# Optimization experiments

Hardware: AMD Instinct MI355X
Metric: run time of the kernel (lower is better)

## Reference

```python
import jax, jax.numpy as jnp
import numpy as np

DIM = 192
NUM_HEADS = 6
WS = (7, 7, 7)
N_TOK = WS[0] * WS[1] * WS[2]  # 343
TABLE_SIZE = (2 * WS[0] - 1) * (2 * WS[1] - 1) * (2 * WS[2] - 1)  # 2197


def _relative_position_index():
    # faithful replication of the torch buffer construction (incl. its strides)
    coords = np.stack(np.meshgrid(np.arange(WS[0]), np.arange(WS[1]), np.arange(WS[2]), indexing='ij'))
    flat = coords.reshape(3, -1)                     # [3, N]
    rel = flat[:, :, None] - flat[:, None, :]        # [3, N, N]
    rel = rel.transpose(1, 2, 0).astype(np.int64)    # [N, N, 3]
    rel[..., 0] += WS[0] - 1
    rel[..., 1] += WS[1] - 1
    rel[..., 2] += WS[2] - 1
    rel[..., 0] *= 3 * WS[1] - 1  # = 20 (source uses window_size[1] here)
    rel[..., 1] *= 2 * WS[1] - 1  # = 13
    return rel.sum(-1)            # [N, N]


def setup_inputs() -> dict:
    key = jax.random.key(0)
    ks = jax.random.split(key, 10)
    B_, nW = 256, 64
    x1 = jax.random.normal(ks[0], (B_, N_TOK, DIM), dtype=jnp.float32)
    x2 = jax.random.normal(ks[1], (B_, N_TOK, DIM), dtype=jnp.float32)
    mask = jax.random.normal(ks[2], (nW, N_TOK, N_TOK), dtype=jnp.float32)
    table = 0.02 * jax.random.normal(ks[3], (TABLE_SIZE, NUM_HEADS), dtype=jnp.float32)
    s = DIM ** -0.5
    q_w = s * jax.random.normal(ks[4], (DIM, DIM), dtype=jnp.float32)
    q_b = jnp.zeros((DIM,), jnp.float32)
    kv_w = s * jax.random.normal(ks[5], (2 * DIM, DIM), dtype=jnp.float32)
    kv_b = jnp.zeros((2 * DIM,), jnp.float32)
    proj_w = s * jax.random.normal(ks[6], (DIM, DIM), dtype=jnp.float32)
    proj_b = jnp.zeros((DIM,), jnp.float32)
    rel_idx = jnp.asarray(_relative_position_index(), dtype=jnp.int32)
    return {"x1": x1, "x2": x2, "mask": mask, "table": table,
            "q_w": q_w, "q_b": q_b, "kv_w": kv_w, "kv_b": kv_b,
            "proj_w": proj_w, "proj_b": proj_b, "rel_idx": rel_idx}


def reference(x1, x2, mask, table, q_w, q_b, kv_w, kv_b, proj_w, proj_b, rel_idx):
    B_, N, C = x1.shape
    H = NUM_HEADS
    hd = C // H
    scale = hd ** -0.5
    # q from x1, k/v from x2 (isfusion cross-attention path)
    q = (x1 @ q_w.T + q_b).reshape(B_, N, H, hd).transpose(0, 2, 1, 3) * scale  # [B,H,N,hd]
    kv = (x2 @ kv_w.T + kv_b).reshape(B_, N, 2, H, hd).transpose(2, 0, 3, 1, 4)  # [2,B,H,N,hd]
    k, v = kv[0], kv[1]
    attn = jnp.einsum('bhnd,bhmd->bhnm', q, k)  # [B,H,N,N]
    # relative position bias gather -> [H,N,N]
    bias = table[rel_idx.reshape(-1)].reshape(N, N, H).transpose(2, 0, 1)
    attn = attn + bias[None]
    # shifted-window mask add
    nW = mask.shape[0]
    attn = (attn.reshape(B_ // nW, nW, H, N, N) + mask[None, :, None]).reshape(B_, H, N, N)
    attn = jax.nn.softmax(attn, axis=-1)
    out = jnp.einsum('bhnm,bhmd->bnhd', attn, v).reshape(B_, N, C)
    return out @ proj_w.T + proj_b
```

## Files before the change

### kernel.cpp

```cpp
#include <hip/hip_runtime.h>

typedef __attribute__((ext_vector_type(8))) short short8;
typedef __attribute__((ext_vector_type(4))) float f32x4;
typedef __attribute__((ext_vector_type(16))) float f32x16;
typedef __attribute__((ext_vector_type(4))) unsigned short us4;
typedef __attribute__((ext_vector_type(2))) unsigned int u32x2;

#define NTOK 343
#define BMP 352
#define LOG2E 1.4426950408889634f
#define FPLANE 11264
#define WPITCH 200

#define OFF_QG   0u
#define OFF_KG   33718272u
#define OFF_VT   68321280u
#define OFF_AO   102924288u
#define OFF_WB   136642560u

__device__ __forceinline__ unsigned short f2bf(float f) {
  union { float f; unsigned u; } v; v.f = f;
  unsigned r = v.u + 0x7FFFu + ((v.u >> 16) & 1u);
  return (unsigned short)(r >> 16);
}

__device__ __forceinline__ float bf2f(unsigned short b) {
  union { unsigned u; float f; } v; v.u = ((unsigned)b) << 16;
  return v.f;
}

__device__ __forceinline__ short8 ld8(const unsigned short* p) {
  return *reinterpret_cast<const short8*>(p);
}

__device__ __forceinline__ float fexp2(float x) {
  float r; asm("v_exp_f32 %0, %1" : "=v"(r) : "v"(x)); return r;
}

__device__ __forceinline__ unsigned cvtpk(float a, float b) {
  unsigned r; asm("v_cvt_pk_bf16_f32 %0, %1, %2" : "=v"(r) : "v"(a), "v"(b)); return r;
}

__device__ __forceinline__ void plswap(unsigned &a, unsigned &b) {
  asm("v_permlane32_swap_b32 %0, %1" : "+v"(a), "+v"(b));
}

__device__ __forceinline__ f32x16 mfma32(short8 a, short8 b, f32x16 c) {
  return __builtin_amdgcn_mfma_f32_32x32x16_bf16(a, b, c, 0, 0, 0);
}

__device__ __forceinline__ f32x4 mfma16(short8 a, short8 b, f32x4 c) {
  return __builtin_amdgcn_mfma_f32_16x16x32_bf16(a, b, c, 0, 0, 0);
}

union frag_u { unsigned u[4]; short8 s8; };

__global__ __launch_bounds__(256) void precompute(
    const float* __restrict__ x1, const float* __restrict__ x2,
    const float* __restrict__ mask, const float* __restrict__ table,
    const int* __restrict__ rel_idx,
    const float* __restrict__ qw, const float* __restrict__ kvw, const float* __restrict__ pw,
    unsigned short* __restrict__ x1b, unsigned short* __restrict__ x2b,
    unsigned short* __restrict__ wq_bf, unsigned short* __restrict__ wkv_bf,
    unsigned short* __restrict__ wp_bf,
    unsigned short* __restrict__ bias_bf, unsigned short* __restrict__ mask_bf,
    unsigned short* __restrict__ v_frag)
{
  const int idx = blockIdx.x * 256 + threadIdx.x;
  if (idx < 8429568) {
    const float* src; unsigned short* dst; int i;
    if (idx < 4214784) { src = x1; dst = x1b; i = idx; }
    else               { src = x2; dst = x2b; i = idx - 4214784; }
    f32x4 v = *reinterpret_cast<const f32x4*>(src + i * 4);
    us4 o; o[0] = f2bf(v[0]); o[1] = f2bf(v[1]); o[2] = f2bf(v[2]); o[3] = f2bf(v[3]);
    *reinterpret_cast<us4*>(dst + i * 4) = o;
  } else if (idx < 8466432) {
    const int wi = idx - 8429568;
    const float* src; unsigned short* dst; int i;
    if (wi < 9216)       { src = qw;  dst = wq_bf;  i = wi; }
    else if (wi < 27648) { src = kvw; dst = wkv_bf; i = wi - 9216; }
    else                 { src = pw;  dst = wp_bf;  i = wi - 27648; }
    f32x4 v = *reinterpret_cast<const f32x4*>(src + i * 4);
    us4 o; o[0] = f2bf(v[0]); o[1] = f2bf(v[1]); o[2] = f2bf(v[2]); o[3] = f2bf(v[3]);
    *reinterpret_cast<us4*>(dst + i * 4) = o;
  } else if (idx < 10398208) {
    const int mi = idx - 8466432;
    const int row = mi / 88, q = mi - row * 88;
    const int j0 = q * 4;
    unsigned short* dst = mask_bf + row * BMP + j0;
    if (q < 85) {
      const float* src = mask + row * NTOK + j0;
      us4 o; o[0] = f2bf(LOG2E * src[0]); o[1] = f2bf(LOG2E * src[1]);
      o[2] = f2bf(LOG2E * src[2]); o[3] = f2bf(LOG2E * src[3]);
      *reinterpret_cast<us4*>(dst) = o;
    } else {
      us4 o;
      #pragma unroll
      for (int i = 0; i < 4; ++i) {
        const int col = j0 + i;
        o[i] = (col < NTOK) ? f2bf(LOG2E * mask[row * NTOK + col]) : (unsigned short)0;
      }
      *reinterpret_cast<us4*>(dst) = o;
    }
  } else if (idx < 10515857) {
    const int i = idx - 10398208;
    const int ri = rel_idx[i] * 6;
    const int rrow = i / NTOK, j = i - rrow * NTOK;
    unsigned short* dst = bias_bf + rrow * BMP + j;
    #pragma unroll
    for (int h = 0; h < 6; ++h) dst[h * (NTOK * BMP)] = f2bf(LOG2E * table[ri + h]);
  } else if (idx < 10517915) {
    const int p = idx - 10515857;
    unsigned short* dst = bias_bf + p * BMP + NTOK;
    #pragma unroll
    for (int c = 0; c < 9; ++c) dst[c] = 0;
  } else if (idx < 10714523) {
    const int i = idx - 10517915;
    const int bh = i >> 7, c = i & 127;
    short8 z = (short8){0,0,0,0,0,0,0,0};
    *reinterpret_cast<short8*>(v_frag + bh * FPLANE + 10240 + c * 8) = z;
  }
}

__global__ __launch_bounds__(256) void proj(
    const unsigned short* __restrict__ x1b, const unsigned short* __restrict__ x2b,
    const unsigned short* __restrict__ wq_bf, const unsigned short* __restrict__ wkv_bf,
    const float* __restrict__ qb, const float* __restrict__ kvb,
    unsigned short* __restrict__ q_g, unsigned short* __restrict__ k_g,
    unsigned short* __restrict__ v_frag)
{
  __shared__ __align__(16) unsigned short wLds[192 * WPITCH];

  const int tid = threadIdx.x;
  const int wv = tid >> 6, lane = tid & 63, lg = lane >> 4, lr = lane & 15;
  const int path = blockIdx.y;
  const int b = blockIdx.x & 255, seg = blockIdx.x >> 8;
  const int n0 = seg * 128 + wv * 32;

  const unsigned short* X = (path == 0) ? x1b : x2b;
  const unsigned short* Wsrc = (path == 0) ? wq_bf : (path == 1 ? wkv_bf : wkv_bf + 36864);

  #pragma unroll
  for (int i = 0; i < 18; ++i) {
    const int c = i * 256 + tid;
    const int row = c / 24, c8 = c - row * 24;
    *reinterpret_cast<short8*>(&wLds[row * WPITCH + c8 * 8]) = ld8(Wsrc + row * 192 + c8 * 8);
  }
  __syncthreads();

  const int rowbase = b * NTOK;
  const int nA = n0 + lr, nB = n0 + 16 + lr;
  const unsigned short* xr0 = X + (rowbase + (nA < NTOK ? nA : NTOK - 1)) * 192 + lg * 8;
  const unsigned short* xr1 = X + (rowbase + (nB < NTOK ? nB : NTOK - 1)) * 192 + lg * 8;

  short8 ax[2][6];
  #pragma unroll
  for (int kk = 0; kk < 6; ++kk) {
    ax[0][kk] = ld8(xr0 + kk * 32);
    ax[1][kk] = ld8(xr1 + kk * 32);
  }

  f32x4 acc[2][12];
  #pragma unroll
  for (int i = 0; i < 2; ++i)
    #pragma unroll
    for (int j = 0; j < 12; ++j) acc[i][j] = (f32x4){0.f, 0.f, 0.f, 0.f};

  if (path < 2) {
    #pragma unroll
    for (int kk = 0; kk < 6; ++kk) {
      const int k0 = kk * 32 + lg * 8;
      #pragma unroll
      for (int ct = 0; ct < 12; ++ct) {
        const short8 wf = *reinterpret_cast<const short8*>(&wLds[(ct * 16 + lr) * WPITCH + k0]);
        acc[0][ct] = mfma16(wf, ax[0][kk], acc[0][ct]);
        acc[1][ct] = mfma16(wf, ax[1][kk], acc[1][ct]);
      }
    }
    if (path == 0) {
      const float qs = 0.17677669529663687f * LOG2E;
      #pragma unroll
      for (int tt = 0; tt < 2; ++tt) {
        const int n = n0 + tt * 16 + lr;
        if (n < NTOK) {
          unsigned short* ob = q_g + (b * 6 * NTOK + n) * 32;
          #pragma unroll
          for (int ct = 0; ct < 12; ++ct) {
            const f32x4 bb = *reinterpret_cast<const f32x4*>(qb + ct * 16 + lg * 4);
            u32x2 pk;
            pk[0] = cvtpk((acc[tt][ct][0] + bb[0]) * qs, (acc[tt][ct][1] + bb[1]) * qs);
            pk[1] = cvtpk((acc[tt][ct][2] + bb[2]) * qs, (acc[tt][ct][3] + bb[3]) * qs);
            *reinterpret_cast<u32x2*>(ob + (ct >> 1) * (NTOK * 32) + (ct & 1) * 16 + lg * 4) = pk;
          }
        }
      }
    } else {
      #pragma unroll
      for (int tt = 0; tt < 2; ++tt) {
        const int n = n0 + tt * 16 + lr;
        if (n < 352) {
          unsigned short* ob = k_g + b * 6 * FPLANE + (n >> 5) * 1024
                               + ((lg >> 1) * 32 + (n & 31)) * 8 + (lg & 1) * 4;
          #pragma unroll
          for (int ct = 0; ct < 12; ++ct) {
            const f32x4 bb = *reinterpret_cast<const f32x4*>(kvb + ct * 16 + lg * 4);
            u32x2 pk;
            pk[0] = cvtpk(acc[tt][ct][0] + bb[0], acc[tt][ct][1] + bb[1]);
            pk[1] = cvtpk(acc[tt][ct][2] + bb[2], acc[tt][ct][3] + bb[3]);
            *reinterpret_cast<u32x2*>(ob + (ct >> 1) * FPLANE + (ct & 1) * 512) = pk;
          }
        }
      }
    }
  } else {
    #pragma unroll
    for (int kk = 0; kk < 6; ++kk) {
      const int k0 = kk * 32 + lg * 8;
      #pragma unroll
      for (int ct = 0; ct < 12; ++ct) {
        const short8 wf = *reinterpret_cast<const short8*>(&wLds[(ct * 16 + lr) * WPITCH + k0]);
        acc[0][ct] = mfma16(ax[0][kk], wf, acc[0][ct]);
        acc[1][ct] = mfma16(ax[1][kk], wf, acc[1][ct]);
      }
    }
    float bs[12];
    #pragma unroll
    for (int ct = 0; ct < 12; ++ct) bs[ct] = kvb[192 + ct * 16 + lr];
    #pragma unroll
    for (int tt = 0; tt < 2; ++tt) {
      const int nb = n0 + tt * 16 + lg * 4;
      if (nb < 352) {
        unsigned short* vb = v_frag + b * 6 * FPLANE + (nb >> 5) * 1024
                             + ((nb >> 4) & 1) * 512 + ((nb >> 3) & 1) * 256 + (nb & 7);
        #pragma unroll
        for (int ct = 0; ct < 12; ++ct) {
          const int d = (ct & 1) * 16 + lr;
          u32x2 pk;
          pk[0] = cvtpk(acc[tt][ct][0] + bs[ct], acc[tt][ct][1] + bs[ct]);
          pk[1] = cvtpk(acc[tt][ct][2] + bs[ct], acc[tt][ct][3] + bs[ct]);
          *reinterpret_cast<u32x2*>(vb + (ct >> 1) * FPLANE + d * 8) = pk;
        }
      }
    }
  }
}

__global__ __launch_bounds__(256, 3) void attn(
    const unsigned short* __restrict__ q_g, const unsigned short* __restrict__ k_g,
    const unsigned short* __restrict__ v_frag, const unsigned short* __restrict__ bias_bf,
    const unsigned short* __restrict__ mask_bf, unsigned short* __restrict__ attn_out)
{
  __shared__ __align__(16) unsigned short kvlds[2][FPLANE];

  const int tid = threadIdx.x;
  const int wv = tid >> 6, lane = tid & 63;
  const int l31 = lane & 31, hi = lane >> 5;
  const int s0 = blockIdx.x;
  const int xcd = s0 & 7, ii = s0 >> 3;
  const int g = xcd * 48 + (ii >> 2), mem = ii & 3;
  const int h = g >> 6, w = g & 63;
  const int b = mem * 64 + w;
  const int bid = b * 6 + h;

  const unsigned short* qp = q_g + bid * (NTOK * 32);
  const unsigned short* kpf = k_g + bid * FPLANE;
  const unsigned short* vpf = v_frag + bid * FPLANE;
  const unsigned short* bias_h = bias_bf + h * (NTOK * BMP);
  const unsigned short* mask_w = mask_bf + w * (NTOK * BMP);

  #pragma unroll
  for (int j = 0; j < 6; ++j) {
    const int c = j * 256 + tid;
    if (c < 1408) {
      *reinterpret_cast<short8*>(&kvlds[0][c * 8]) = ld8(kpf + c * 8);
      *reinterpret_cast<short8*>(&kvlds[1][c * 8]) = ld8(vpf + c * 8);
    }
  }
  __syncthreads();

  for (int qt = wv; qt < 11; qt += 4) {
    const int qq = qt * 32 + l31;
    const int qrc = qq < NTOK ? qq : NTOK - 1;
    const short8 qf0 = ld8(qp + qrc * 32 + hi * 8);
    const short8 qf1 = ld8(qp + qrc * 32 + 16 + hi * 8);
    const unsigned short* bmb = bias_h + qrc * BMP + hi * 4;
    const unsigned short* bmm = mask_w + qrc * BMP + hi * 4;

    f32x16 O;
    #pragma unroll
    for (int r = 0; r < 16; ++r) O[r] = 0.f;
    f32x4 sacc = (f32x4){0.f, 0.f, 0.f, 0.f};

    us4 nb[4], nm[4];
    #pragma unroll
    for (int gg = 0; gg < 4; ++gg) {
      nb[gg] = *reinterpret_cast<const us4*>(bmb + gg * 8);
      nm[gg] = *reinterpret_cast<const us4*>(bmm + gg * 8);
    }

    #pragma unroll
    for (int kt = 0; kt < 11; ++kt) {
      us4 cb[4], cm[4];
      #pragma unroll
      for (int gg = 0; gg < 4; ++gg) { cb[gg] = nb[gg]; cm[gg] = nm[gg]; }
      if (kt < 10) {
        const int kn = (kt + 1) * 32;
        #pragma unroll
        for (int gg = 0; gg < 4; ++gg) {
          nb[gg] = *reinterpret_cast<const us4*>(bmb + kn + gg * 8);
          nm[gg] = *reinterpret_cast<const us4*>(bmm + kn + gg * 8);
        }
      }

      const short8 kf0 = ld8(&kvlds[0][kt * 1024 + lane * 8]);
      const short8 kf1 = ld8(&kvlds[0][kt * 1024 + 512 + lane * 8]);
      f32x16 sv;
      #pragma unroll
      for (int r = 0; r < 16; ++r) sv[r] = 0.f;
      __builtin_amdgcn_s_setprio(1);
      sv = mfma32(kf0, qf0, sv);
      sv = mfma32(kf1, qf1, sv);
      __builtin_amdgcn_s_setprio(0);

      float p[16];
      #pragma unroll
      for (int gg = 0; gg < 4; ++gg) {
        #pragma unroll
        for (int j = 0; j < 4; ++j) {
          float v = sv[gg * 4 + j] + (bf2f(cb[gg][j]) + bf2f(cm[gg][j]));
          if (kt == 10 && (gg * 8 + hi * 4 + j) >= 23) v = -3.0e38f;
          p[gg * 4 + j] = fexp2(v);
        }
      }
      #pragma unroll
      for (int j = 0; j < 4; ++j)
        sacc[j] += (p[j] + p[4 + j]) + (p[8 + j] + p[12 + j]);

      unsigned c01 = cvtpk(p[0], p[1]),   c23 = cvtpk(p[2], p[3]);
      unsigned c45 = cvtpk(p[4], p[5]),   c67 = cvtpk(p[6], p[7]);
      unsigned d01 = cvtpk(p[8], p[9]),   d23 = cvtpk(p[10], p[11]);
      unsigned d45 = cvtpk(p[12], p[13]), d67 = cvtpk(p[14], p[15]);
      plswap(c01, c45); plswap(c23, c67);
      plswap(d01, d45); plswap(d23, d67);
      frag_u P0, P1;
      P0.u[0] = c01; P0.u[1] = c23; P0.u[2] = c45; P0.u[3] = c67;
      P1.u[0] = d01; P1.u[1] = d23; P1.u[2] = d45; P1.u[3] = d67;

      const short8 vf0 = ld8(&kvlds[1][kt * 1024 + lane * 8]);
      const short8 vf1 = ld8(&kvlds[1][kt * 1024 + 512 + lane * 8]);
      __builtin_amdgcn_s_setprio(1);
      O = mfma32(vf0, P0.s8, O);
      O = mfma32(vf1, P1.s8, O);
      __builtin_amdgcn_s_setprio(0);
    }

    float sum = (sacc[0] + sacc[1]) + (sacc[2] + sacc[3]);
    sum += __shfl_xor(sum, 32);
    const float inv = 1.0f / sum;
    if (qq < NTOK) {
      unsigned short* op = attn_out + (b * NTOK + qq) * 192 + h * 32;
      #pragma unroll
      for (int gg = 0; gg < 4; ++gg) {
        us4 ov;
        #pragma unroll
        for (int j = 0; j < 4; ++j) ov[j] = f2bf(O[gg * 4 + j] * inv);
        *reinterpret_cast<us4*>(op + gg * 8 + hi * 4) = ov;
      }
    }
  }
}

__global__ __launch_bounds__(256) void proj_out(
    const unsigned short* __restrict__ a_in, const unsigned short* __restrict__ wp_bf,
    const float* __restrict__ pb, float* __restrict__ out)
{
  __shared__ __align__(16) unsigned short wLds[192 * WPITCH];

  const int tid = threadIdx.x;
  const int wv = tid >> 6, lane = tid & 63, lg = lane >> 4, lr = lane & 15;
  const int t0 = blockIdx.x * 128 + wv * 32;

  #pragma unroll
  for (int i = 0; i < 18; ++i) {
    const int c = i * 256 + tid;
    const int row = c / 24, c8 = c - row * 24;
    *reinterpret_cast<short8*>(&wLds[row * WPITCH + c8 * 8]) = ld8(wp_bf + row * 192 + c8 * 8);
  }
  __syncthreads();

  const unsigned short* xr0 = a_in + (t0 + lr) * 192 + lg * 8;
  const unsigned short* xr1 = xr0 + 16 * 192;

  short8 ax[2][6];
  #pragma unroll
  for (int kk = 0; kk < 6; ++kk) {
    ax[0][kk] = ld8(xr0 + kk * 32);
    ax[1][kk] = ld8(xr1 + kk * 32);
  }

  f32x4 acc[2][12];
  #pragma unroll
  for (int i = 0; i < 2; ++i)
    #pragma unroll
    for (int j = 0; j < 12; ++j) acc[i][j] = (f32x4){0.f, 0.f, 0.f, 0.f};

  #pragma unroll
  for (int kk = 0; kk < 6; ++kk) {
    const int k0 = kk * 32 + lg * 8;
    #pragma unroll
    for (int ct = 0; ct < 12; ++ct) {
      const short8 wf = *reinterpret_cast<const short8*>(&wLds[(ct * 16 + lr) * WPITCH + k0]);
      acc[0][ct] = mfma16(wf, ax[0][kk], acc[0][ct]);
      acc[1][ct] = mfma16(wf, ax[1][kk], acc[1][ct]);
    }
  }

  #pragma unroll
  for (int tt = 0; tt < 2; ++tt) {
    const int t = t0 + tt * 16 + lr;
    float* op = out + t * 192 + lg * 4;
    #pragma unroll
    for (int ct = 0; ct < 12; ++ct) {
      const f32x4 bb = *reinterpret_cast<const f32x4*>(pb + ct * 16 + lg * 4);
      f32x4 ov;
      #pragma unroll
      for (int r = 0; r < 4; ++r) ov[r] = acc[tt][ct][r] + bb[r];
      *reinterpret_cast<f32x4*>(op + ct * 16) = ov;
    }
  }
}

extern "C" void kernel_launch(void* const* d_in, const int* in_sizes, int n_in,
                              void* d_out, int out_size, void* d_ws, size_t ws_size,
                              hipStream_t stream) {
  const float* x1    = (const float*)d_in[0];
  const float* x2    = (const float*)d_in[1];
  const float* mask  = (const float*)d_in[2];
  const float* table = (const float*)d_in[3];
  const float* qw    = (const float*)d_in[4];
  const float* qb    = (const float*)d_in[5];
  const float* kvw   = (const float*)d_in[6];
  const float* kvb   = (const float*)d_in[7];
  const float* pw    = (const float*)d_in[8];
  const float* pb    = (const float*)d_in[9];
  const int* rel_idx = (const int*)d_in[10];

  char* ws = (char*)d_ws;
  char* outc = (char*)d_out;
  unsigned short* q_g     = (unsigned short*)(ws + OFF_QG);
  unsigned short* k_g     = (unsigned short*)(ws + OFF_KG);
  unsigned short* v_frag  = (unsigned short*)(ws + OFF_VT);
  unsigned short* a_o     = (unsigned short*)(ws + OFF_AO);
  unsigned short* wq_bf   = (unsigned short*)(ws + OFF_WB);
  unsigned short* wkv_bf  = wq_bf + 36864;
  unsigned short* wp_bf   = wkv_bf + 73728;
  unsigned short* x1b     = a_o;
  unsigned short* x2b     = (unsigned short*)outc;
  unsigned short* bias_bf = (unsigned short*)(outc + 33718272);
  unsigned short* mask_bf = (unsigned short*)(outc + 35167104);

  hipLaunchKernelGGL(precompute, dim3(41854), dim3(256), 0, stream,
                     x1, x2, mask, table, rel_idx, qw, kvw, pw,
                     x1b, x2b, wq_bf, wkv_bf, wp_bf, bias_bf, mask_bf, v_frag);
  hipLaunchKernelGGL(proj, dim3(768, 3), dim3(256), 0, stream,
                     x1b, x2b, wq_bf, wkv_bf, qb, kvb, q_g, k_g, v_frag);
  hipLaunchKernelGGL(attn, dim3(1536), dim3(256), 0, stream,
                     q_g, k_g, v_frag, bias_bf, mask_bf, a_o);
  hipLaunchKernelGGL(proj_out, dim3(686), dim3(256), 0, stream,
                     a_o, wp_bf, pb, (float*)d_out);
}
```

Baseline: 226.8 us.

## Fuse fp32-to-bf16 input conversion into projection and widen attention blocks to six waves

The separate pass that converted x1/x2 to bf16 in the precompute kernel is removed. The projection kernel now loads fp32 inputs directly and packs them to bf16 in registers, which avoids writing and re-reading a bf16 copy of both activations. Separately, the attention kernel moves from 256 to 384 threads (6 waves), so its 11 query tiles are spread over 6 waves instead of 4. The launch bound also changes to (384, 4), which raises register pressure risk, and the proj kernel now reads twice as many input bytes.

```diff
diff --git a/kernel.cpp b/kernel.cpp
--- a/kernel.cpp
+++ b/kernel.cpp
@@ -55,27 +55,27 @@
 
 union frag_u { unsigned u[4]; short8 s8; };
 
+__device__ __forceinline__ short8 cvt8f(const float* p) {
+  f32x4 a = *reinterpret_cast<const f32x4*>(p);
+  f32x4 b = *reinterpret_cast<const f32x4*>(p + 4);
+  frag_u f;
+  f.u[0] = cvtpk(a[0], a[1]); f.u[1] = cvtpk(a[2], a[3]);
+  f.u[2] = cvtpk(b[0], b[1]); f.u[3] = cvtpk(b[2], b[3]);
+  return f.s8;
+}
+
 __global__ __launch_bounds__(256) void precompute(
-    const float* __restrict__ x1, const float* __restrict__ x2,
     const float* __restrict__ mask, const float* __restrict__ table,
     const int* __restrict__ rel_idx,
     const float* __restrict__ qw, const float* __restrict__ kvw, const float* __restrict__ pw,
-    unsigned short* __restrict__ x1b, unsigned short* __restrict__ x2b,
     unsigned short* __restrict__ wq_bf, unsigned short* __restrict__ wkv_bf,
     unsigned short* __restrict__ wp_bf,
     unsigned short* __restrict__ bias_bf, unsigned short* __restrict__ mask_bf,
     unsigned short* __restrict__ v_frag)
 {
   const int idx = blockIdx.x * 256 + threadIdx.x;
-  if (idx < 8429568) {
-    const float* src; unsigned short* dst; int i;
-    if (idx < 4214784) { src = x1; dst = x1b; i = idx; }
-    else               { src = x2; dst = x2b; i = idx - 4214784; }
-    f32x4 v = *reinterpret_cast<const f32x4*>(src + i * 4);
-    us4 o; o[0] = f2bf(v[0]); o[1] = f2bf(v[1]); o[2] = f2bf(v[2]); o[3] = f2bf(v[3]);
-    *reinterpret_cast<us4*>(dst + i * 4) = o;
-  } else if (idx < 8466432) {
-    const int wi = idx - 8429568;
+  if (idx < 36864) {
+    const int wi = idx;
     const float* src; unsigned short* dst; int i;
     if (wi < 9216)       { src = qw;  dst = wq_bf;  i = wi; }
     else if (wi < 27648) { src = kvw; dst = wkv_bf; i = wi - 9216; }
@@ -83,8 +83,8 @@
     f32x4 v = *reinterpret_cast<const f32x4*>(src + i * 4);
     us4 o; o[0] = f2bf(v[0]); o[1] = f2bf(v[1]); o[2] = f2bf(v[2]); o[3] = f2bf(v[3]);
     *reinterpret_cast<us4*>(dst + i * 4) = o;
-  } else if (idx < 10398208) {
-    const int mi = idx - 8466432;
+  } else if (idx < 1968640) {
+    const int mi = idx - 36864;
     const int row = mi / 88, q = mi - row * 88;
     const int j0 = q * 4;
     unsigned short* dst = mask_bf + row * BMP + j0;
@@ -102,20 +102,20 @@
       }
       *reinterpret_cast<us4*>(dst) = o;
     }
-  } else if (idx < 10515857) {
-    const int i = idx - 10398208;
+  } else if (idx < 2086289) {
+    const int i = idx - 1968640;
     const int ri = rel_idx[i] * 6;
     const int rrow = i / NTOK, j = i - rrow * NTOK;
     unsigned short* dst = bias_bf + rrow * BMP + j;
     #pragma unroll
     for (int h = 0; h < 6; ++h) dst[h * (NTOK * BMP)] = f2bf(LOG2E * table[ri + h]);
-  } else if (idx < 10517915) {
-    const int p = idx - 10515857;
+  } else if (idx < 2088347) {
+    const int p = idx - 2086289;
     unsigned short* dst = bias_bf + p * BMP + NTOK;
     #pragma unroll
     for (int c = 0; c < 9; ++c) dst[c] = 0;
-  } else if (idx < 10714523) {
-    const int i = idx - 10517915;
+  } else if (idx < 2284955) {
+    const int i = idx - 2088347;
     const int bh = i >> 7, c = i & 127;
     short8 z = (short8){0,0,0,0,0,0,0,0};
     *reinterpret_cast<short8*>(v_frag + bh * FPLANE + 10240 + c * 8) = z;
@@ -123,7 +123,7 @@
 }
 
 __global__ __launch_bounds__(256) void proj(
-    const unsigned short* __restrict__ x1b, const unsigned short* __restrict__ x2b,
+    const float* __restrict__ x1f, const float* __restrict__ x2f,
     const unsigned short* __restrict__ wq_bf, const unsigned short* __restrict__ wkv_bf,
     const float* __restrict__ qb, const float* __restrict__ kvb,
     unsigned short* __restrict__ q_g, unsigned short* __restrict__ k_g,
@@ -137,7 +137,7 @@
   const int b = blockIdx.x & 255, seg = blockIdx.x >> 8;
   const int n0 = seg * 128 + wv * 32;
 
-  const unsigned short* X = (path == 0) ? x1b : x2b;
+  const float* X = (path == 0) ? x1f : x2f;
   const unsigned short* Wsrc = (path == 0) ? wq_bf : (path == 1 ? wkv_bf : wkv_bf + 36864);
 
   #pragma unroll
@@ -150,14 +150,14 @@
 
   const int rowbase = b * NTOK;
   const int nA = n0 + lr, nB = n0 + 16 + lr;
-  const unsigned short* xr0 = X + (rowbase + (nA < NTOK ? nA : NTOK - 1)) * 192 + lg * 8;
-  const unsigned short* xr1 = X + (rowbase + (nB < NTOK ? nB : NTOK - 1)) * 192 + lg * 8;
+  const float* xr0 = X + (rowbase + (nA < NTOK ? nA : NTOK - 1)) * 192 + lg * 8;
+  const float* xr1 = X + (rowbase + (nB < NTOK ? nB : NTOK - 1)) * 192 + lg * 8;
 
   short8 ax[2][6];
   #pragma unroll
   for (int kk = 0; kk < 6; ++kk) {
-    ax[0][kk] = ld8(xr0 + kk * 32);
-    ax[1][kk] = ld8(xr1 + kk * 32);
+    ax[0][kk] = cvt8f(xr0 + kk * 32);
+    ax[1][kk] = cvt8f(xr1 + kk * 32);
   }
 
   f32x4 acc[2][12];
@@ -245,7 +245,7 @@
   }
 }
 
-__global__ __launch_bounds__(256, 3) void attn(
+__global__ __launch_bounds__(384, 4) void attn(
     const unsigned short* __restrict__ q_g, const unsigned short* __restrict__ k_g,
     const unsigned short* __restrict__ v_frag, const unsigned short* __restrict__ bias_bf,
     const unsigned short* __restrict__ mask_bf, unsigned short* __restrict__ attn_out)
@@ -269,8 +269,8 @@
   const unsigned short* mask_w = mask_bf + w * (NTOK * BMP);
 
   #pragma unroll
-  for (int j = 0; j < 6; ++j) {
-    const int c = j * 256 + tid;
+  for (int j = 0; j < 4; ++j) {
+    const int c = j * 384 + tid;
     if (c < 1408) {
       *reinterpret_cast<short8*>(&kvlds[0][c * 8]) = ld8(kpf + c * 8);
       *reinterpret_cast<short8*>(&kvlds[1][c * 8]) = ld8(vpf + c * 8);
@@ -278,7 +278,7 @@
   }
   __syncthreads();
 
-  for (int qt = wv; qt < 11; qt += 4) {
+  for (int qt = wv; qt < 11; qt += 6) {
     const int qq = qt * 32 + l31;
     const int qrc = qq < NTOK ? qq : NTOK - 1;
     const short8 qf0 = ld8(qp + qrc * 32 + hi * 8);
@@ -454,17 +454,15 @@
   unsigned short* wq_bf   = (unsigned short*)(ws + OFF_WB);
   unsigned short* wkv_bf  = wq_bf + 36864;
   unsigned short* wp_bf   = wkv_bf + 73728;
-  unsigned short* x1b     = a_o;
-  unsigned short* x2b     = (unsigned short*)outc;
   unsigned short* bias_bf = (unsigned short*)(outc + 33718272);
   unsigned short* mask_bf = (unsigned short*)(outc + 35167104);
 
-  hipLaunchKernelGGL(precompute, dim3(41854), dim3(256), 0, stream,
-                     x1, x2, mask, table, rel_idx, qw, kvw, pw,
-                     x1b, x2b, wq_bf, wkv_bf, wp_bf, bias_bf, mask_bf, v_frag);
+  hipLaunchKernelGGL(precompute, dim3(8926), dim3(256), 0, stream,
+                     mask, table, rel_idx, qw, kvw, pw,
+                     wq_bf, wkv_bf, wp_bf, bias_bf, mask_bf, v_frag);
   hipLaunchKernelGGL(proj, dim3(768, 3), dim3(256), 0, stream,
-                     x1b, x2b, wq_bf, wkv_bf, qb, kvb, q_g, k_g, v_frag);
-  hipLaunchKernelGGL(attn, dim3(1536), dim3(256), 0, stream,
+                     x1, x2, wq_bf, wkv_bf, qb, kvb, q_g, k_g, v_frag);
+  hipLaunchKernelGGL(attn, dim3(1536), dim3(384), 0, stream,
                      q_g, k_g, v_frag, bias_bf, mask_bf, a_o);
   hipLaunchKernelGGL(proj_out, dim3(686), dim3(256), 0, stream,
                      a_o, wp_bf, pb, (float*)d_out);
```

Measured after the change: 223.1 us. No clear change (-1.6%).
